# Performance work log

Measured on AMD Instinct MI355X. Metric: run time of the kernel, lower is better.

The kernel has to match this reference:

```python
import jax, jax.numpy as jnp
import numpy as np

N = 10000        # nodes
E = 160000       # edges (avg degree 16)
C = 64           # hidden channels
L = 2            # interaction/product/readout blocks
NTYPES = 5       # len(atomic_numbers)
NB = 8           # Bessel radial basis size
G = 100          # graphs in batch
R_MAX = 5.0
AVG_NEI = 16.0   # avg_num_neighbors normalization
LM = 9           # (l_max+1)^2, l_max=2


def _spherical_harmonics(u):
    # real spherical harmonics up to l=2 of unit vectors u [E,3] -> [E,9]
    x, y, z = u[:, 0], u[:, 1], u[:, 2]
    s3 = 1.7320508
    one = jnp.ones_like(x)
    return jnp.stack([
        one,                       # l=0
        x, y, z,                   # l=1
        s3 * x * y,                # l=2
        s3 * y * z,
        0.5 * (3.0 * z * z - 1.0),
        s3 * x * z,
        0.5 * s3 * (x * x - y * y),
    ], axis=-1)


def _radial_embedding(r):
    # Bessel basis * polynomial cutoff (p=6); r [E] -> [E,NB]
    r_safe = jnp.maximum(r, 1e-9)
    n = jnp.arange(1, NB + 1, dtype=r.dtype)
    pref = jnp.sqrt(jnp.asarray(2.0 / R_MAX, r.dtype))
    bessel = pref * jnp.sin(n[None, :] * jnp.pi * r[:, None] / R_MAX) / r_safe[:, None]
    xx = r / R_MAX
    env = 1.0 - 28.0 * xx**6 + 48.0 * xx**7 - 21.0 * xx**8
    env = jnp.where(xx < 1.0, env, 0.0)
    return bessel * env[:, None]


def setup_inputs() -> dict:
    key = jax.random.key(0)
    ks = jax.random.split(key, 14)
    sc = 0.1
    return {
        'pos': jax.random.normal(ks[0], (N, 3), jnp.float32),
        'W_embed': jax.random.normal(ks[1], (NTYPES, C), jnp.float32) * sc,
        'W_r1': jax.random.normal(ks[2], (NB, 64), jnp.float32) * sc,
        'b_r1': jnp.zeros((64,), jnp.float32),
        'W_r2': jax.random.normal(ks[3], (64, C), jnp.float32) * sc,
        'W_up': jax.random.normal(ks[4], (L, C, C), jnp.float32) * sc,
        'W_sc': jax.random.normal(ks[5], (L, C, C), jnp.float32) * sc,
        'W_prod': jax.random.normal(ks[6], (L, C, C), jnp.float32) * sc,
        'w_ro': jax.random.normal(ks[7], (L, C, 1), jnp.float32) * sc,
        'atom_types': jax.random.randint(ks[8], (N,), 0, NTYPES),
        'edge_index': jax.random.randint(ks[9], (2, E), 0, N),
        'batch': jnp.sort(jax.random.randint(ks[10], (N,), 0, G)),
        'num_graphs': G,
    }


def reference(pos, W_embed, W_r1, b_r1, W_r2, W_up, W_sc, W_prod, w_ro,
              atom_types, edge_index, batch, num_graphs):
    node_attrs = jax.nn.one_hot(atom_types, NTYPES, dtype=pos.dtype)   # [N,5]
    h = node_attrs @ W_embed                                           # [N,C]

    sender, receiver = edge_index[0], edge_index[1]
    vec = pos[receiver] - pos[sender]                                  # edge gather
    r = jnp.linalg.norm(vec, axis=-1)                                  # [E]
    u = vec / jnp.maximum(r, 1e-9)[:, None]
    sh = _spherical_harmonics(u)                                       # [E,LM]
    ef = _radial_embedding(r)                                          # [E,NB]
    R = jax.nn.silu(ef @ W_r1 + b_r1) @ W_r2                            # [E,C] radial MLP

    pair_energy = jnp.zeros((num_graphs,), pos.dtype)                  # no pair_repulsion_fn
    energies = [pair_energy]
    for l in range(L):
        h1 = h @ W_up[l]                                               # [N,C]
        # tensor-product message: outer(sh_e, R_e * h_sender)  [E,LM,C]
        m = sh[:, :, None] * (R * h1[sender])[:, None, :]
        A = jax.ops.segment_sum(m, receiver, num_segments=N) / AVG_NEI  # [N,LM,C]
        sc = h @ W_sc[l]                                               # skip connection
        # product basis: l=0 channel + quadratic invariant contraction
        q = A[:, 0, :] + jnp.sum(A * A, axis=1)                         # [N,C]
        h = q @ W_prod[l] + sc
        node_e = (h @ w_ro[l])[:, 0]                                    # [N]
        energies.append(jax.ops.segment_sum(node_e, batch, num_segments=num_graphs))

    contributions = jnp.stack(energies, axis=-1)                        # [G, L+1]
    total_energy = jnp.sum(contributions, axis=-1)                      # [G]
    return total_energy
```

## Files before the change

### kernel.cpp

```cpp
#include <hip/hip_runtime.h>
#include <hip/hip_fp16.h>
#include <math.h>

#define Nn 10000
#define Ee 160000
#define NBb 8
#define Gg 100
#define NT 5
#define CSRMAX 230400
#define EDGEBLK (CSRMAX / 256)

typedef _Float16 half8v __attribute__((ext_vector_type(8)));
typedef float f32x4v __attribute__((ext_vector_type(4)));

__device__ __align__(16) float g_shc[(size_t)CSRMAX * 12];
__device__ __align__(16) __half2 g_R2[(size_t)(CSRMAX / 2) * 64];
__device__ float g_h1b[Nn * 64];
__device__ float g_hscb[Nn * 64];
__device__ float g_nodeE[2][Nn];
__device__ int   g_deg[Nn];
__device__ int   g_offs[Nn + 1];
__device__ int   g_cursor[Nn];
__device__ int2  g_er[CSRMAX];
__device__ float g_W1T[64 * NBb];
__device__ float g_E1[NT * 64];
__device__ float g_Esc[NT * 64];
__device__ float g_T1[NT * 64];
__device__ float g_T2[NT * 64];
__device__ float g_M12[64 * 128];
__device__ float g_wp0ro[64];
__device__ float g_wpro[64];
__device__ float g_t0[NT];

__global__ __launch_bounds__(256) void k_init(const float* __restrict__ Wr1,
                                              const float* __restrict__ Wembed,
                                              const float* __restrict__ Wup,
                                              const float* __restrict__ Wsc,
                                              const float* __restrict__ Wprod,
                                              const float* __restrict__ wro,
                                              float* __restrict__ out, int out_size) {
    int t = threadIdx.x;
    int b = blockIdx.x;
    if (b >= 17) {
        int i = (b - 17) * 256 + t;
        if (i < CSRMAX) g_er[i].x = -1;
        if (i < out_size) out[i] = 0.0f;
        if (i < Nn) { g_deg[i] = 0; g_cursor[i] = 0; }
        return;
    }
    if (b == 0) {
        for (int i = t; i < 64 * NBb; i += 256) {
            int k = i >> 6, j = i & 63;
            g_W1T[j * NBb + k] = Wr1[i];
        }
        for (int i = t; i < NT * 64; i += 256) {
            int g = i >> 6, c = i & 63;
            float s1 = 0.f, s2 = 0.f;
            for (int j = 0; j < 64; j++) {
                float w = Wembed[g * 64 + j];
                s1 += w * Wup[j * 64 + c];
                s2 += w * Wsc[j * 64 + c];
            }
            g_E1[i] = s1; g_Esc[i] = s2;
        }
        if (t < 64) {
            float s1 = 0.f, s2 = 0.f;
            for (int c = 0; c < 64; c++) {
                s1 += Wprod[t * 64 + c] * wro[c];
                s2 += Wprod[4096 + t * 64 + c] * wro[64 + c];
            }
            g_wp0ro[t] = s1; g_wpro[t] = s2;
        }
        __syncthreads();
        for (int i = t; i < NT * 64; i += 256) {
            int g = i >> 6, c = i & 63;
            float s1 = 0.f, s2 = 0.f;
            for (int j = 0; j < 64; j++) {
                float w = g_Esc[g * 64 + j];
                s1 += w * Wup[4096 + j * 64 + c];
                s2 += w * Wsc[4096 + j * 64 + c];
            }
            g_T1[i] = s1; g_T2[i] = s2;
        }
        if (t < NT) {
            float s = 0.f;
            for (int j = 0; j < 64; j++) s += g_Esc[t * 64 + j] * wro[j];
            g_t0[t] = s;
        }
    } else {
        int idx = (b - 1) * 256 + t;
        int k = idx >> 6, c = idx & 63;
        float s1 = 0.f, s2 = 0.f;
        for (int j = 0; j < 64; j++) {
            float w = Wprod[k * 64 + j];
            s1 += w * Wup[4096 + j * 64 + c];
            s2 += w * Wsc[4096 + j * 64 + c];
        }
        g_M12[k * 128 + c] = s1;
        g_M12[k * 128 + 64 + c] = s2;
    }
}

__global__ __launch_bounds__(256) void k_deg(const int* __restrict__ eidx) {
    int e = blockIdx.x * 256 + threadIdx.x;
    if (e < Ee) atomicAdd(&g_deg[eidx[Ee + e]], 1);
}

__global__ __launch_bounds__(1024) void k_scan() {
    __shared__ int part[1024];
    int t = threadIdx.x;
    const int CH = (Nn + 1023) / 1024;
    int st = t * CH;
    int en = st + CH; if (en > Nn) en = Nn;
    int s = 0;
    for (int i = st; i < en; i++) s += (g_deg[i] + 7) & ~7;
    part[t] = s;
    __syncthreads();
    for (int d = 1; d < 1024; d <<= 1) {
        int v = (t >= d) ? part[t - d] : 0;
        __syncthreads();
        part[t] += v;
        __syncthreads();
    }
    int base = (t == 0) ? 0 : part[t - 1];
    for (int i = st; i < en; i++) { g_offs[i] = base; base += (g_deg[i] + 7) & ~7; }
    if (t == 1023) g_offs[Nn] = part[1023];
}

__global__ __launch_bounds__(256) void k_fill(const int* __restrict__ eidx) {
    int e = blockIdx.x * 256 + threadIdx.x;
    if (e >= Ee) return;
    int snd = eidx[e];
    int r = eidx[Ee + e];
    int p = g_offs[r] + atomicAdd(&g_cursor[r], 1);
    g_er[p] = make_int2(snd, r);
}

__global__ __launch_bounds__(256) void k_edge(const float* __restrict__ pos,
                                              const float* __restrict__ br1,
                                              const float* __restrict__ Wr2,
                                              const int* __restrict__ atom_types) {
    int t = threadIdx.x;
    __shared__ _Float16 sA[256 * 64];
    __shared__ _Float16 sB[64 * 64];
    int total = g_offs[Nn];
    if (blockIdx.x * 256 >= total) return;

    for (int i = t; i < 64 * 64; i += 256)
        sB[(i & 63) * 64 + (i >> 6)] = (_Float16)Wr2[i];

    int s = blockIdx.x * 256 + t;
    int2 er = g_er[s];
    bool real = (er.x >= 0);
    int snd = real ? er.x : 0;
    int rcv = real ? er.y : 0;
    int stype = atom_types[snd];

    float vx = pos[3 * rcv + 0] - pos[3 * snd + 0];
    float vy = pos[3 * rcv + 1] - pos[3 * snd + 1];
    float vz = pos[3 * rcv + 2] - pos[3 * snd + 2];
    float r = sqrtf(vx * vx + vy * vy + vz * vz);
    float inv = __builtin_amdgcn_rcpf(fmaxf(r, 1e-9f));
    float x = vx * inv, y = vy * inv, z = vz * inv;
    const float s3 = 1.7320508f;
    {
        float4* shp = (float4*)(g_shc + (size_t)s * 12);
        if (real) {
            shp[0] = make_float4(1.0f, x, y, z);
            shp[1] = make_float4(s3 * x * y, s3 * y * z, 0.5f * (3.0f * z * z - 1.0f), s3 * x * z);
            shp[2] = make_float4(0.5f * s3 * (x * x - y * y), __int_as_float(snd),
                                 __int_as_float(stype), 0.f);
        } else {
            shp[0] = make_float4(0.f, 0.f, 0.f, 0.f);
            shp[1] = make_float4(0.f, 0.f, 0.f, 0.f);
            shp[2] = make_float4(0.f, 0.f, 0.f, 0.f);
        }
    }

    float xx = r * 0.2f;
    float env = 0.0f;
    if (xx < 1.0f) {
        float x2 = xx * xx;
        float x6 = x2 * x2 * x2;
        float x7 = x6 * xx;
        float x8 = x7 * xx;
        env = 1.0f - 28.0f * x6 + 48.0f * x7 - 21.0f * x8;
    }
    const float pref = 0.63245553f;
    const float PI_F = 3.14159265358979f;
    float fac = pref * inv * env;
    float ef[NBb];
#pragma unroll
    for (int k = 0; k < NBb; k++)
        ef[k] = fac * __sinf((float)(k + 1) * PI_F * r * 0.2f);

#pragma unroll
    for (int gnl = 0; gnl < 8; gnl++) {
        half8v h8;
#pragma unroll
        for (int i2 = 0; i2 < 8; i2++) {
            int j = gnl * 8 + i2;
            float a = br1[j];
#pragma unroll
            for (int k = 0; k < NBb; k++) a += ef[k] * g_W1T[j * NBb + k];
            a = a * __builtin_amdgcn_rcpf(1.0f + __expf(-a));
            h8[i2] = (_Float16)(real ? a : 0.0f);
        }
        int pg = gnl ^ (t & 7);
        *(half8v*)&sA[t * 64 + pg * 8] = h8;
    }
    __syncthreads();

    int lane = t & 63;
    int w = t >> 6;
    half8v Bf[4][2];
#pragma unroll
    for (int n = 0; n < 4; n++) {
#pragma unroll
        for (int kk = 0; kk < 2; kk++) {
            int c = n * 16 + (lane & 15);
            int j0 = kk * 32 + (lane >> 4) * 8;
            Bf[n][kk] = *(const half8v*)&sB[c * 64 + j0];
        }
    }
#pragma unroll
    for (int m = 0; m < 4; m++) {
        int row = w * 64 + m * 16 + (lane & 15);
        int q0 = (lane >> 4) ^ (lane & 7);
        int q1 = (4 + (lane >> 4)) ^ (lane & 7);
        half8v A0 = *(const half8v*)&sA[row * 64 + q0 * 8];
        half8v A1 = *(const half8v*)&sA[row * 64 + q1 * 8];
        size_t pairbase = (size_t)blockIdx.x * 128 + (size_t)w * 32 + m * 8 + (lane >> 4) * 2;
        int cbase = lane & 15;
#pragma unroll
        for (int n = 0; n < 4; n++) {
            f32x4v d = {0.f, 0.f, 0.f, 0.f};
            d = __builtin_amdgcn_mfma_f32_16x16x32_f16(A0, Bf[n][0], d, 0, 0, 0);
            d = __builtin_amdgcn_mfma_f32_16x16x32_f16(A1, Bf[n][1], d, 0, 0, 0);
            int c = n * 16 + cbase;
            g_R2[pairbase * 64 + c]       = __floats2half2_rn(d[0], d[1]);
            g_R2[(pairbase + 1) * 64 + c] = __floats2half2_rn(d[2], d[3]);
        }
    }
}

#define NODE_BATCH_E1(j0)                                                        \
    {                                                                            \
        const float* __restrict__ rp = g_shc + (size_t)(j0) * 12;                \
        __half2 r2t[4];                                                          \
        _Pragma("unroll")                                                        \
        for (int kk = 0; kk < 4; kk++)                                           \
            r2t[kk] = g_R2[((j0) / 2 + kk) * 64 + lane];                         \
        float s8v[8]; int stv[8];                                                \
        _Pragma("unroll")                                                        \
        for (int k = 0; k < 8; k++) {                                            \
            float4 rc = *(const float4*)(rp + k * 12 + 8);                       \
            s8v[k] = rc.x; stv[k] = __float_as_int(rc.z);                        \
        }                                                                        \
        float hv[8];                                                             \
        _Pragma("unroll")                                                        \
        for (int k = 0; k < 8; k++)                                              \
            hv[k] = g_E1[stv[k] * 64 + lane];                                    \
        _Pragma("unroll")                                                        \
        for (int k = 0; k < 8; k++) {                                            \
            float4 ra = *(const float4*)(rp + k * 12);                           \
            float4 rb = *(const float4*)(rp + k * 12 + 4);                       \
            float rv = (k & 1) ? __high2float(r2t[k >> 1]) : __low2float(r2t[k >> 1]); \
            float tv = rv * hv[k];                                               \
            A[0] += ra.x * tv; A[1] += ra.y * tv; A[2] += ra.z * tv;             \
            A[3] += ra.w * tv; A[4] += rb.x * tv; A[5] += rb.y * tv;             \
            A[6] += rb.z * tv; A[7] += rb.w * tv; A[8] += s8v[k] * tv;           \
        }                                                                        \
    }

#define NODE_BATCH(j0)                                                           \
    {                                                                            \
        const float* __restrict__ rp = g_shc + (size_t)(j0) * 12;                \
        __half2 r2t[4];                                                          \
        _Pragma("unroll")                                                        \
        for (int kk = 0; kk < 4; kk++)                                           \
            r2t[kk] = g_R2[((j0) / 2 + kk) * 64 + lane];                         \
        float s8v[8]; int srcv[8];                                               \
        _Pragma("unroll")                                                        \
        for (int k = 0; k < 8; k++) {                                            \
            float2 rc = *(const float2*)(rp + k * 12 + 8);                       \
            s8v[k] = rc.x; srcv[k] = __float_as_int(rc.y);                       \
        }                                                                        \
        float hv[8];                                                             \
        _Pragma("unroll")                                                        \
        for (int k = 0; k < 8; k++)                                              \
            hv[k] = hsrc[(size_t)srcv[k] * 64 + lane];                           \
        _Pragma("unroll")                                                        \
        for (int k = 0; k < 8; k++) {                                            \
            float4 ra = *(const float4*)(rp + k * 12);                           \
            float4 rb = *(const float4*)(rp + k * 12 + 4);                       \
            float rv = (k & 1) ? __high2float(r2t[k >> 1]) : __low2float(r2t[k >> 1]); \
            float tv = rv * hv[k];                                               \
            A[0] += ra.x * tv; A[1] += ra.y * tv; A[2] += ra.z * tv;             \
            A[3] += ra.w * tv; A[4] += rb.x * tv; A[5] += rb.y * tv;             \
            A[6] += rb.z * tv; A[7] += rb.w * tv; A[8] += s8v[k] * tv;           \
        }                                                                        \
    }

__global__ __launch_bounds__(256) void k_node0(const int* __restrict__ atom_types) {
    int t = threadIdx.x;
    int node = blockIdx.x * 4 + (t >> 6);
    int lane = t & 63;
    int boff = __builtin_amdgcn_readfirstlane(g_offs[node]);
    int nb = (__builtin_amdgcn_readfirstlane(g_deg[node]) + 7) >> 3;
    float A[9];
#pragma unroll
    for (int m = 0; m < 9; m++) A[m] = 0.0f;
#pragma unroll
    for (int b = 0; b < 4; b++)
        if (b < nb) NODE_BATCH_E1((size_t)boff + (size_t)b * 8);
    for (int b = 4; b < nb; b++) {
        size_t j0 = (size_t)boff + (size_t)b * 8;
        NODE_BATCH_E1(j0);
    }
    const float invn = 1.0f / 16.0f;
    float q = A[0] * invn;
#pragma unroll
    for (int m = 0; m < 9; m++) {
        float a = A[m] * invn;
        q += a * a;
    }
    int type = __builtin_amdgcn_readfirstlane(atom_types[node]);
    float h1n = g_T1[type * 64 + lane];
    float hscn = g_T2[type * 64 + lane];
#pragma unroll
    for (int k = 0; k < 64; k++) {
        float qk = __shfl(q, k, 64);
        h1n += qk * g_M12[k * 128 + lane];
        hscn += qk * g_M12[k * 128 + 64 + lane];
    }
    g_h1b[node * 64 + lane] = h1n;
    g_hscb[node * 64 + lane] = hscn;
    float v = q * g_wp0ro[lane];
#pragma unroll
    for (int off = 32; off > 0; off >>= 1) v += __shfl_down(v, off, 64);
    if (lane == 0) g_nodeE[0][node] = v + g_t0[type];
}

__global__ __launch_bounds__(256) void k_node1(const float* __restrict__ wro) {
    int t = threadIdx.x;
    int node = blockIdx.x * 4 + (t >> 6);
    int lane = t & 63;
    int boff = __builtin_amdgcn_readfirstlane(g_offs[node]);
    int nb = (__builtin_amdgcn_readfirstlane(g_deg[node]) + 7) >> 3;
    const float* __restrict__ hsrc = g_h1b;
    float A[9];
#pragma unroll
    for (int m = 0; m < 9; m++) A[m] = 0.0f;
#pragma unroll
    for (int b = 0; b < 4; b++)
        if (b < nb) NODE_BATCH((size_t)boff + (size_t)b * 8);
    for (int b = 4; b < nb; b++) {
        size_t j0 = (size_t)boff + (size_t)b * 8;
        NODE_BATCH(j0);
    }
    const float invn = 1.0f / 16.0f;
    float q = A[0] * invn;
#pragma unroll
    for (int m = 0; m < 9; m++) {
        float a = A[m] * invn;
        q += a * a;
    }
    float v = q * g_wpro[lane] + g_hscb[node * 64 + lane] * wro[lane];
#pragma unroll
    for (int off = 32; off > 0; off >>= 1) v += __shfl_down(v, off, 64);
    if (lane == 0) g_nodeE[1][node] = v;
}

__global__ __launch_bounds__(64) void k_energy(const int* __restrict__ batch,
                                               float* __restrict__ out) {
    int g = blockIdx.x;
    int lane = threadIdx.x;
    int a = 0, b = Nn;
    while (a < b) { int m = (a + b) >> 1; if (batch[m] < g) a = m + 1; else b = m; }
    int st = a;
    b = Nn;
    while (a < b) { int m = (a + b) >> 1; if (batch[m] < g + 1) a = m + 1; else b = m; }
    int en = a;
    float s = 0.0f;
    for (int i = st + lane; i < en; i += 64) s += g_nodeE[0][i] + g_nodeE[1][i];
#pragma unroll
    for (int off = 32; off > 0; off >>= 1) s += __shfl_down(s, off, 64);
    if (lane == 0) out[g] = s;
}

extern "C" void kernel_launch(void* const* d_in, const int* in_sizes, int n_in,
                              void* d_out, int out_size, void* d_ws, size_t ws_size,
                              hipStream_t stream) {
    const float* pos     = (const float*)d_in[0];
    const float* W_embed = (const float*)d_in[1];
    const float* W_r1    = (const float*)d_in[2];
    const float* b_r1    = (const float*)d_in[3];
    const float* W_r2    = (const float*)d_in[4];
    const float* W_up    = (const float*)d_in[5];
    const float* W_sc    = (const float*)d_in[6];
    const float* W_prod  = (const float*)d_in[7];
    const float* w_ro    = (const float*)d_in[8];
    const int* atom_types = (const int*)d_in[9];
    const int* eidx       = (const int*)d_in[10];
    const int* batch      = (const int*)d_in[11];
    float* out = (float*)d_out;

    k_init<<<17 + EDGEBLK, 256, 0, stream>>>(W_r1, W_embed, W_up, W_sc, W_prod, w_ro, out, out_size);
    k_deg<<<Ee / 256, 256, 0, stream>>>(eidx);
    k_scan<<<1, 1024, 0, stream>>>();
    k_fill<<<Ee / 256, 256, 0, stream>>>(eidx);
    k_edge<<<EDGEBLK, 256, 0, stream>>>(pos, b_r1, W_r2, atom_types);
    k_node0<<<Nn / 4, 256, 0, stream>>>(atom_types);
    k_node1<<<Nn / 4, 256, 0, stream>>>(w_ro + 64);
    k_energy<<<Gg, 64, 0, stream>>>(batch, out);
}
```

Baseline: 186.3 us.

## Fuse node layer kernels and energy reduction into one cooperative persistent kernel

Replaces the three launches (node layer 0, node layer 1, per-graph energy reduction) with a single cooperative kernel. A persistent grid of waves loops over nodes, and grid-wide syncs separate the stages. This removes two kernel launch gaps and the idle tail of each launch. In exchange it adds grid sync costs, limits the grid to resident blocks, and keeps the old three-kernel path as a fallback if the cooperative launch fails.

After: 571.6 us. 207% more time.

```diff
diff --git a/kernel.cpp b/kernel.cpp
--- a/kernel.cpp
+++ b/kernel.cpp
@@ -1,5 +1,6 @@
 #include <hip/hip_runtime.h>
 #include <hip/hip_fp16.h>
+#include <hip/hip_cooperative_groups.h>
 #include <math.h>
 
 #define Nn 10000
@@ -259,8 +260,7 @@
         }                                                                        \
         float hv[8];                                                             \
         _Pragma("unroll")                                                        \
-        for (int k = 0; k < 8; k++)                                              \
-            hv[k] = g_E1[stv[k] * 64 + lane];                                    \
+        for (int k = 0; k < 8; k++) hv[k] = g_E1[stv[k] * 64 + lane];            \
         _Pragma("unroll")                                                        \
         for (int k = 0; k < 8; k++) {                                            \
             float4 ra = *(const float4*)(rp + k * 12);                           \
@@ -387,6 +387,104 @@
 #pragma unroll
     for (int off = 32; off > 0; off >>= 1) s += __shfl_down(s, off, 64);
     if (lane == 0) out[g] = s;
+}
+
+__global__ __launch_bounds__(256, 4) void k_nodes(const int* __restrict__ atom_types,
+                                                  const float* __restrict__ wro1,
+                                                  const int* __restrict__ batch,
+                                                  float* __restrict__ out,
+                                                  int nwaves) {
+    namespace cg = cooperative_groups;
+    cg::grid_group grid = cg::this_grid();
+    int t = threadIdx.x;
+    int lane = t & 63;
+    int w = t >> 6;
+    int wgid = blockIdx.x * 4 + w;
+
+    for (int node = wgid; node < Nn; node += nwaves) {
+        int boff = __builtin_amdgcn_readfirstlane(g_offs[node]);
+        int nb = (__builtin_amdgcn_readfirstlane(g_deg[node]) + 7) >> 3;
+        float A[9];
+#pragma unroll
+        for (int m = 0; m < 9; m++) A[m] = 0.0f;
+#pragma unroll
+        for (int b = 0; b < 4; b++)
+            if (b < nb) NODE_BATCH_E1((size_t)boff + (size_t)b * 8);
+        for (int b = 4; b < nb; b++) {
+            size_t j0 = (size_t)boff + (size_t)b * 8;
+            NODE_BATCH_E1(j0);
+        }
+        const float invn = 1.0f / 16.0f;
+        float q = A[0] * invn;
+#pragma unroll
+        for (int m = 0; m < 9; m++) {
+            float a = A[m] * invn;
+            q += a * a;
+        }
+        int type = __builtin_amdgcn_readfirstlane(atom_types[node]);
+        float h1n = g_T1[type * 64 + lane];
+        float hscn = g_T2[type * 64 + lane];
+#pragma unroll
+        for (int k = 0; k < 64; k++) {
+            float qk = __shfl(q, k, 64);
+            h1n += qk * g_M12[k * 128 + lane];
+            hscn += qk * g_M12[k * 128 + 64 + lane];
+        }
+        g_h1b[node * 64 + lane] = h1n;
+        g_hscb[node * 64 + lane] = hscn;
+        float v = q * g_wp0ro[lane];
+#pragma unroll
+        for (int off = 32; off > 0; off >>= 1) v += __shfl_down(v, off, 64);
+        if (lane == 0) g_nodeE[0][node] = v + g_t0[type];
+    }
+    __threadfence();
+    grid.sync();
+    __threadfence();
+
+    for (int node = wgid; node < Nn; node += nwaves) {
+        int boff = __builtin_amdgcn_readfirstlane(g_offs[node]);
+        int nb = (__builtin_amdgcn_readfirstlane(g_deg[node]) + 7) >> 3;
+        const float* __restrict__ hsrc = g_h1b;
+        float A[9];
+#pragma unroll
+        for (int m = 0; m < 9; m++) A[m] = 0.0f;
+#pragma unroll
+        for (int b = 0; b < 4; b++)
+            if (b < nb) NODE_BATCH((size_t)boff + (size_t)b * 8);
+        for (int b = 4; b < nb; b++) {
+            size_t j0 = (size_t)boff + (size_t)b * 8;
+            NODE_BATCH(j0);
+        }
+        const float invn = 1.0f / 16.0f;
+        float q = A[0] * invn;
+#pragma unroll
+        for (int m = 0; m < 9; m++) {
+            float a = A[m] * invn;
+            q += a * a;
+        }
+        float v = q * g_wpro[lane] + g_hscb[node * 64 + lane] * wro1[lane];
+#pragma unroll
+        for (int off = 32; off > 0; off >>= 1) v += __shfl_down(v, off, 64);
+        if (lane == 0) g_nodeE[1][node] = v;
+    }
+    __threadfence();
+    grid.sync();
+    __threadfence();
+
+    if (wgid < Gg) {
+        int g = wgid;
+        int a = 0, b = Nn;
+        while (a < b) { int m = (a + b) >> 1; if (batch[m] < g) a = m + 1; else b = m; }
+        int st = a;
+        b = Nn;
+        while (a < b) { int m = (a + b) >> 1; if (batch[m] < g + 1) a = m + 1; else b = m; }
+        int en = a;
+        float s = 0.0f;
+        for (int i = st + lane; i < en; i += 64) s += g_nodeE[0][i] + g_nodeE[1][i];
+#pragma unroll
+        for (int off = 32; off > 0; off >>= 1) s += __shfl_down(s, off, 64);
+        if (lane == 0) out[g] = s;
+    }
 }
 
 extern "C" void kernel_launch(void* const* d_in, const int* in_sizes, int n_in,
@@ -411,7 +509,20 @@
     k_scan<<<1, 1024, 0, stream>>>();
     k_fill<<<Ee / 256, 256, 0, stream>>>(eidx);
     k_edge<<<EDGEBLK, 256, 0, stream>>>(pos, b_r1, W_r2, atom_types);
-    k_node0<<<Nn / 4, 256, 0, stream>>>(atom_types);
-    k_node1<<<Nn / 4, 256, 0, stream>>>(w_ro + 64);
-    k_energy<<<Gg, 64, 0, stream>>>(batch, out);
-}
+
+    const float* wro1 = w_ro + 64;
+    int maxB = 0;
+    hipError_t oe = hipOccupancyMaxActiveBlocksPerMultiprocessor(&maxB, k_nodes, 256, 0);
+    int nblk = (oe == hipSuccess && maxB > 0) ? (maxB * 256) : 768;
+    if (nblk > 960) nblk = 960;
+    int nwaves = nblk * 4;
+    void* args[] = { (void*)&atom_types, (void*)&wro1, (void*)&batch, (void*)&out,
+                     (void*)&nwaves };
+    hipError_t e = hipLaunchCooperativeKernel((const void*)k_nodes, dim3(nblk), dim3(256),
+                                              args, 0, stream);
+    if (e != hipSuccess) {
+        k_node0<<<Nn / 4, 256, 0, stream>>>(atom_types);
+        k_node1<<<Nn / 4, 256, 0, stream>>>(w_ro + 64);
+        k_energy<<<Gg, 64, 0, stream>>>(batch, out);
+    }
+}
```

## Pack spherical harmonics as fp16 and fuse graph energy reduction via atomics

Applied to the files above, without the earlier changes.

Each edge record drops from 12 to 8 floats: the eight non-constant spherical harmonic values are stored as packed fp16 and the constant l=0 term is implied, which cuts the bytes streamed per edge in both node kernels. The separate k_energy kernel and the g_nodeE buffer are removed, and each node wave atomically adds its energy into the per-graph output. This saves one launch and one pass over the node energies. In exchange it loses harmonic precision and makes the summation order non-deterministic; it also relies on k_init zeroing the output, which the code before appears to do.

After: 259.4 us. 39.2% more time.

```diff
diff --git a/kernel.cpp b/kernel.cpp
--- a/kernel.cpp
+++ b/kernel.cpp
@@ -13,11 +13,10 @@
 typedef _Float16 half8v __attribute__((ext_vector_type(8)));
 typedef float f32x4v __attribute__((ext_vector_type(4)));
 
-__device__ __align__(16) float g_shc[(size_t)CSRMAX * 12];
+__device__ __align__(16) float g_shc[(size_t)CSRMAX * 8];
 __device__ __align__(16) __half2 g_R2[(size_t)(CSRMAX / 2) * 64];
 __device__ float g_h1b[Nn * 64];
 __device__ float g_hscb[Nn * 64];
-__device__ float g_nodeE[2][Nn];
 __device__ int   g_deg[Nn];
 __device__ int   g_offs[Nn + 1];
 __device__ int   g_cursor[Nn];
@@ -164,16 +163,18 @@
     float x = vx * inv, y = vy * inv, z = vz * inv;
     const float s3 = 1.7320508f;
     {
-        float4* shp = (float4*)(g_shc + (size_t)s * 12);
+        float4* shp = (float4*)(g_shc + (size_t)s * 8);
         if (real) {
-            shp[0] = make_float4(1.0f, x, y, z);
-            shp[1] = make_float4(s3 * x * y, s3 * y * z, 0.5f * (3.0f * z * z - 1.0f), s3 * x * z);
-            shp[2] = make_float4(0.5f * s3 * (x * x - y * y), __int_as_float(snd),
-                                 __int_as_float(stype), 0.f);
+            float4 q0;
+            ((__half2*)&q0)[0] = __floats2half2_rn(x, y);
+            ((__half2*)&q0)[1] = __floats2half2_rn(z, s3 * x * y);
+            ((__half2*)&q0)[2] = __floats2half2_rn(s3 * y * z, 0.5f * (3.0f * z * z - 1.0f));
+            ((__half2*)&q0)[3] = __floats2half2_rn(s3 * x * z, 0.5f * s3 * (x * x - y * y));
+            shp[0] = q0;
+            shp[1] = make_float4(__int_as_float(snd), __int_as_float(stype), 0.f, 0.f);
         } else {
             shp[0] = make_float4(0.f, 0.f, 0.f, 0.f);
             shp[1] = make_float4(0.f, 0.f, 0.f, 0.f);
-            shp[2] = make_float4(0.f, 0.f, 0.f, 0.f);
         }
     }
 
@@ -244,65 +245,58 @@
     }
 }
 
+#define NODE_FMA_LOOP(rp, r2t, hv)                                               \
+    _Pragma("unroll")                                                            \
+    for (int k = 0; k < 8; k++) {                                                \
+        float4 qa = *(const float4*)((rp) + k * 8);                              \
+        const __half2* hp = (const __half2*)&qa;                                 \
+        float2 s12 = __half22float2(hp[0]);                                      \
+        float2 s34 = __half22float2(hp[1]);                                      \
+        float2 s56 = __half22float2(hp[2]);                                      \
+        float2 s78 = __half22float2(hp[3]);                                      \
+        float rv = (k & 1) ? __high2float((r2t)[k >> 1]) : __low2float((r2t)[k >> 1]); \
+        float tv = rv * (hv)[k];                                                 \
+        A[0] += tv;            A[1] += s12.x * tv; A[2] += s12.y * tv;           \
+        A[3] += s34.x * tv;    A[4] += s34.y * tv; A[5] += s56.x * tv;           \
+        A[6] += s56.y * tv;    A[7] += s78.x * tv; A[8] += s78.y * tv;           \
+    }
+
 #define NODE_BATCH_E1(j0)                                                        \
     {                                                                            \
-        const float* __restrict__ rp = g_shc + (size_t)(j0) * 12;                \
+        const float* __restrict__ rp = g_shc + (size_t)(j0) * 8;                 \
         __half2 r2t[4];                                                          \
         _Pragma("unroll")                                                        \
         for (int kk = 0; kk < 4; kk++)                                           \
             r2t[kk] = g_R2[((j0) / 2 + kk) * 64 + lane];                         \
-        float s8v[8]; int stv[8];                                                \
-        _Pragma("unroll")                                                        \
-        for (int k = 0; k < 8; k++) {                                            \
-            float4 rc = *(const float4*)(rp + k * 12 + 8);                       \
-            s8v[k] = rc.x; stv[k] = __float_as_int(rc.z);                        \
-        }                                                                        \
+        int stv[8];                                                              \
+        _Pragma("unroll")                                                        \
+        for (int k = 0; k < 8; k++) stv[k] = __float_as_int(rp[k * 8 + 5]);      \
         float hv[8];                                                             \
         _Pragma("unroll")                                                        \
-        for (int k = 0; k < 8; k++)                                              \
-            hv[k] = g_E1[stv[k] * 64 + lane];                                    \
-        _Pragma("unroll")                                                        \
-        for (int k = 0; k < 8; k++) {                                            \
-            float4 ra = *(const float4*)(rp + k * 12);                           \
-            float4 rb = *(const float4*)(rp + k * 12 + 4);                       \
-            float rv = (k & 1) ? __high2float(r2t[k >> 1]) : __low2float(r2t[k >> 1]); \
-            float tv = rv * hv[k];                                               \
-            A[0] += ra.x * tv; A[1] += ra.y * tv; A[2] += ra.z * tv;             \
-            A[3] += ra.w * tv; A[4] += rb.x * tv; A[5] += rb.y * tv;             \
-            A[6] += rb.z * tv; A[7] += rb.w * tv; A[8] += s8v[k] * tv;           \
-        }                                                                        \
+        for (int k = 0; k < 8; k++) hv[k] = g_E1[stv[k] * 64 + lane];            \
+        NODE_FMA_LOOP(rp, r2t, hv)                                               \
     }
 
 #define NODE_BATCH(j0)                                                           \
     {                                                                            \
-        const float* __restrict__ rp = g_shc + (size_t)(j0) * 12;                \
+        const float* __restrict__ rp = g_shc + (size_t)(j0) * 8;                 \
         __half2 r2t[4];                                                          \
         _Pragma("unroll")                                                        \
         for (int kk = 0; kk < 4; kk++)                                           \
             r2t[kk] = g_R2[((j0) / 2 + kk) * 64 + lane];                         \
-        float s8v[8]; int srcv[8];                                               \
-        _Pragma("unroll")                                                        \
-        for (int k = 0; k < 8; k++) {                                            \
-            float2 rc = *(const float2*)(rp + k * 12 + 8);                       \
-            s8v[k] = rc.x; srcv[k] = __float_as_int(rc.y);                       \
-        }                                                                        \
+        int srcv[8];                                                             \
+        _Pragma("unroll")                                                        \
+        for (int k = 0; k < 8; k++) srcv[k] = __float_as_int(rp[k * 8 + 4]);     \
         float hv[8];                                                             \
         _Pragma("unroll")                                                        \
         for (int k = 0; k < 8; k++)                                              \
             hv[k] = hsrc[(size_t)srcv[k] * 64 + lane];                           \
-        _Pragma("unroll")                                                        \
-        for (int k = 0; k < 8; k++) {                                            \
-            float4 ra = *(const float4*)(rp + k * 12);                           \
-            float4 rb = *(const float4*)(rp + k * 12 + 4);                       \
-            float rv = (k & 1) ? __high2float(r2t[k >> 1]) : __low2float(r2t[k >> 1]); \
-            float tv = rv * hv[k];                                               \
-            A[0] += ra.x * tv; A[1] += ra.y * tv; A[2] += ra.z * tv;             \
-            A[3] += ra.w * tv; A[4] += rb.x * tv; A[5] += rb.y * tv;             \
-            A[6] += rb.z * tv; A[7] += rb.w * tv; A[8] += s8v[k] * tv;           \
-        }                                                                        \
-    }
-
-__global__ __launch_bounds__(256) void k_node0(const int* __restrict__ atom_types) {
+        NODE_FMA_LOOP(rp, r2t, hv)                                               \
+    }
+
+__global__ __launch_bounds__(256) void k_node0(const int* __restrict__ atom_types,
+                                               const int* __restrict__ batch,
+                                               float* __restrict__ out) {
     int t = threadIdx.x;
     int node = blockIdx.x * 4 + (t >> 6);
     int lane = t & 63;
@@ -339,10 +333,12 @@
     float v = q * g_wp0ro[lane];
 #pragma unroll
     for (int off = 32; off > 0; off >>= 1) v += __shfl_down(v, off, 64);
-    if (lane == 0) g_nodeE[0][node] = v + g_t0[type];
-}
-
-__global__ __launch_bounds__(256) void k_node1(const float* __restrict__ wro) {
+    if (lane == 0) atomicAdd(&out[batch[node]], v + g_t0[type]);
+}
+
+__global__ __launch_bounds__(256) void k_node1(const float* __restrict__ wro,
+                                               const int* __restrict__ batch,
+                                               float* __restrict__ out) {
     int t = threadIdx.x;
     int node = blockIdx.x * 4 + (t >> 6);
     int lane = t & 63;
@@ -369,24 +365,7 @@
     float v = q * g_wpro[lane] + g_hscb[node * 64 + lane] * wro[lane];
 #pragma unroll
     for (int off = 32; off > 0; off >>= 1) v += __shfl_down(v, off, 64);
-    if (lane == 0) g_nodeE[1][node] = v;
-}
-
-__global__ __launch_bounds__(64) void k_energy(const int* __restrict__ batch,
-                                               float* __restrict__ out) {
-    int g = blockIdx.x;
-    int lane = threadIdx.x;
-    int a = 0, b = Nn;
-    while (a < b) { int m = (a + b) >> 1; if (batch[m] < g) a = m + 1; else b = m; }
-    int st = a;
-    b = Nn;
-    while (a < b) { int m = (a + b) >> 1; if (batch[m] < g + 1) a = m + 1; else b = m; }
-    int en = a;
-    float s = 0.0f;
-    for (int i = st + lane; i < en; i += 64) s += g_nodeE[0][i] + g_nodeE[1][i];
-#pragma unroll
-    for (int off = 32; off > 0; off >>= 1) s += __shfl_down(s, off, 64);
-    if (lane == 0) out[g] = s;
+    if (lane == 0) atomicAdd(&out[batch[node]], v);
 }
 
 extern "C" void kernel_launch(void* const* d_in, const int* in_sizes, int n_in,
@@ -411,7 +390,6 @@
     k_scan<<<1, 1024, 0, stream>>>();
     k_fill<<<Ee / 256, 256, 0, stream>>>(eidx);
     k_edge<<<EDGEBLK, 256, 0, stream>>>(pos, b_r1, W_r2, atom_types);
-    k_node0<<<Nn / 4, 256, 0, stream>>>(atom_types);
-    k_node1<<<Nn / 4, 256, 0, stream>>>(w_ro + 64);
-    k_energy<<<Gg, 64, 0, stream>>>(batch, out);
-}
+    k_node0<<<Nn / 4, 256, 0, stream>>>(atom_types, batch, out);
+    k_node1<<<Nn / 4, 256, 0, stream>>>(w_ro + 64, batch, out);
+}
```
